# Kernel tuning notes

Measured on AMD Instinct MI355X. Metric: run time of the kernel, lower is better.

Reference implementation:

```python
import jax, jax.numpy as jnp
import numpy as np

TOPK = 8
N_EXPERTS = 64
ROUTE_SCALE = 1.0


def setup_inputs() -> dict:
    key = jax.random.key(0)
    k1, k2 = jax.random.split(key)
    x = jax.random.normal(k1, (16, 256, 64, 64), dtype=jnp.float32)
    gate_w = jax.random.normal(k2, (64, 256, 3, 3), dtype=jnp.float32) * 0.02  # [E, C, kh, kw]
    bias = jnp.zeros((64,), dtype=jnp.float32)  # load-balancing bias buffer
    return {"x": x, "gate_w": gate_w, "bias": bias}


def reference(x, gate_w, bias):
    # 3x3 conv, stride 1, pad 1 (SAME), no conv bias -> expert logits [B, E, H, W]
    logits = jax.lax.conv_general_dilated(
        x, gate_w, window_strides=(1, 1), padding="SAME",
        dimension_numbers=("NCHW", "OIHW", "NCHW"))
    scores = jax.nn.sigmoid(logits)                 # [B, E, H, W]
    s = jnp.moveaxis(scores, 1, -1)                 # [B, H, W, E]
    biased = s + bias                               # bias broadcast over experts
    _, idx = jax.lax.top_k(biased, TOPK)            # [B, H, W, K] (topk on biased scores)
    w = jnp.take_along_axis(s, idx, axis=-1)        # gather UNbiased scores
    w = jax.nn.softmax(w, axis=-1) * ROUTE_SCALE    # softmax over the K selected experts
    weights = jnp.moveaxis(w, -1, 1)                # [B, K, H, W] to match torch layout
    indices = jnp.moveaxis(idx, -1, 1)              # [B, K, H, W]
    counts = jnp.zeros((N_EXPERTS,), jnp.int32).at[idx.ravel()].add(1)  # bincount
    return weights, indices, counts
```

## Files before the change

### kernel.cpp

```cpp
#include <hip/hip_runtime.h>


typedef _Float16 half8 __attribute__((ext_vector_type(8)));
typedef __attribute__((ext_vector_type(4))) float f32x4;

#define LOG2E 1.44269504f

__device__ __forceinline__ unsigned short f2h_bits(float f) {
    _Float16 h = (_Float16)f;
    unsigned short b;
    __builtin_memcpy(&b, &h, 2);
    return b;
}

constexpr int WB_U4 = 8 * 9 * 4 * 64;

__global__ __launch_bounds__(256) void gate_prep(const float* __restrict__ gw,
                                                 unsigned short* __restrict__ wB,
                                                 float* __restrict__ out) {
    int g = blockIdx.x * 256 + threadIdx.x;
    if (blockIdx.x == 0 && threadIdx.x < 64) out[1048576 + threadIdx.x] = 0.f;
    if (g >= WB_U4) return;
    int lane = g & 63;
    int nt   = (g >> 6) & 3;
    int rest = g >> 8;
    int t = rest % 9, q = rest / 9;
    int e  = nt * 16 + (lane & 15);
    int c0 = q * 32 + (lane >> 4) * 8;
    unsigned short o[8];
#pragma unroll
    for (int j = 0; j < 8; ++j)
        o[j] = f2h_bits(gw[(e * 256 + c0 + j) * 9 + t]);
    uint4 pk;
    pk.x = (unsigned)o[0] | ((unsigned)o[1] << 16);
    pk.y = (unsigned)o[2] | ((unsigned)o[3] << 16);
    pk.z = (unsigned)o[4] | ((unsigned)o[5] << 16);
    pk.w = (unsigned)o[6] | ((unsigned)o[7] << 16);
    ((uint4*)wB)[g] = pk;
}

constexpr int CSTR = 40;
constexpr int SLAB = 3 * 66 * CSTR;
constexpr int SSTR = 68;

__global__ __launch_bounds__(256, 4) void gate_main(
    const float* __restrict__ x, const float* __restrict__ bias,
    const unsigned short* __restrict__ wB, float* __restrict__ out) {
    __shared__ unsigned short xs[2 * SLAB];
    __shared__ float bias_s[64];
    __shared__ int   hist[64];

    const int tid  = threadIdx.x;
    const int lane = tid & 63;
    const int rw   = tid >> 6;
    const int blk  = blockIdx.x;
    const int b    = blk & 15;
    const int r    = blk >> 4;

    if (tid < 64) { bias_s[tid] = bias[tid]; hist[tid] = 0; }

    {
        uint4 z = {0u, 0u, 0u, 0u};
        uint4* p = (uint4*)xs;
#pragma unroll
        for (int i = 0; i < 8; ++i) {
            int idx = tid + i * 256;
            if (idx < 2 * SLAB / 8) p[idx] = z;
        }
    }

    bool tOk[4];
    int  tSrc[4], tDst[4];
#pragma unroll
    for (int i = 0; i < 4; ++i) {
        int T = tid + i * 256;
        bool ex = (T < 792);
        int chh = T / 198, s = T - chh * 198;
        int row2 = s / 66, wp = s - row2 * 66;
        int gr = r - 1 + row2, gwc = wp - 1;
        tOk[i]  = ex && (gr >= 0) && (gr < 64) && (gwc >= 0) && (gwc < 64);
        tSrc[i] = ((b * 256 + chh * 8) * 64 + gr) * 64 + gwc;
        tDst[i] = (row2 * 66 + wp) * CSTR + chh * 8;
    }

    float tb[4][8];
    auto issueT = [&](int i, int dq) {
        if (tOk[i]) {
            const float* p = x + tSrc[i] + dq * 131072;
#pragma unroll
            for (int u = 0; u < 8; ++u) tb[i][u] = p[u * 4096];
        }
    };
    auto commitT = [&](int i, unsigned short* dst) {
        if (tOk[i]) {
            uint4 pk;
            pk.x = (unsigned)f2h_bits(tb[i][0]) | ((unsigned)f2h_bits(tb[i][1]) << 16);
            pk.y = (unsigned)f2h_bits(tb[i][2]) | ((unsigned)f2h_bits(tb[i][3]) << 16);
            pk.z = (unsigned)f2h_bits(tb[i][4]) | ((unsigned)f2h_bits(tb[i][5]) << 16);
            pk.w = (unsigned)f2h_bits(tb[i][6]) | ((unsigned)f2h_bits(tb[i][7]) << 16);
            *(uint4*)(dst + tDst[i]) = pk;
        }
    };

    const int ph = rw >> 1, eh = rw & 1;
    half8 Aa[3][2];
    uint4 Bb[3][2];
    auto prefA = [&](const unsigned short* buf, int t, int slot) {
        const int kh = t / 3, kw = t % 3;
        const unsigned short* abase =
            buf + (kh * 66 + ph * 32 + (lane & 15) + kw) * CSTR + (lane >> 4) * 8;
#pragma unroll
        for (int mt = 0; mt < 2; ++mt)
            Aa[slot][mt] = *(const half8*)(abase + mt * 16 * CSTR);
    };
    auto prefB = [&](int T9, int slot) {
        const uint4* bp = (const uint4*)wB + (T9 * 4 + eh * 2) * 64 + lane;
#pragma unroll
        for (int nt = 0; nt < 2; ++nt) Bb[slot][nt] = bp[nt * 64];
    };

    f32x4 acc[2][2];
#pragma unroll
    for (int mt = 0; mt < 2; ++mt)
#pragma unroll
        for (int nt = 0; nt < 2; ++nt) acc[mt][nt] = (f32x4){0.f, 0.f, 0.f, 0.f};

    auto mfma_tap = [&](int slot) {
#pragma unroll
        for (int nt = 0; nt < 2; ++nt) {
            half8 bfr;
            __builtin_memcpy(&bfr, &Bb[slot][nt], 16);
#pragma unroll
            for (int mt = 0; mt < 2; ++mt)
                acc[mt][nt] = __builtin_amdgcn_mfma_f32_16x16x32_f16(
                    Aa[slot][mt], bfr, acc[mt][nt], 0, 0, 0);
        }
    };

    __syncthreads();

    issueT(0, 0); issueT(1, 0); issueT(2, 0); issueT(3, 0);
    commitT(0, xs); commitT(1, xs); commitT(2, xs); commitT(3, xs);
    issueT(0, 1); issueT(1, 1); issueT(2, 1); issueT(3, 1);
    prefB(0, 0); prefB(1, 1); prefB(2, 2);
    __syncthreads();

#pragma unroll 1
    for (int q = 0; q < 8; ++q) {
        const unsigned short* cur = xs + (q & 1) * SLAB;
        unsigned short*       nxt = xs + ((q + 1) & 1) * SLAB;
        const int  T0  = q * 9;
        const bool cmt = (q < 7);
        const bool iss = (q < 6);

        prefA(cur, 0, 0); prefA(cur, 1, 1);
        if (cmt) { commitT(0, nxt); commitT(1, nxt); commitT(2, nxt); commitT(3, nxt); }
        mfma_tap(0); prefB(T0 + 3, 0); prefA(cur, 2, 2);
        mfma_tap(1); prefB(T0 + 4, 1); prefA(cur, 3, 0);
        mfma_tap(2); prefB(T0 + 5, 2); prefA(cur, 4, 1);
        mfma_tap(0); prefB(T0 + 6, 0); prefA(cur, 5, 2);
        mfma_tap(1); prefB(T0 + 7, 1); prefA(cur, 6, 0);
        mfma_tap(2); prefB(T0 + 8, 2); prefA(cur, 7, 1);
        __builtin_amdgcn_sched_barrier(0);
        if (iss) { issueT(0, q + 2); issueT(1, q + 2); issueT(2, q + 2); issueT(3, q + 2); }
        __builtin_amdgcn_sched_barrier(0);
        mfma_tap(0); if (cmt) prefB(T0 + 9, 0);  prefA(cur, 8, 2);
        mfma_tap(1); if (cmt) prefB(T0 + 10, 1);
        mfma_tap(2); if (cmt) prefB(T0 + 11, 2);
        __syncthreads();
    }

    float* scf = (float*)xs;
#pragma unroll
    for (int mt = 0; mt < 2; ++mt)
#pragma unroll
        for (int nt = 0; nt < 2; ++nt)
#pragma unroll
            for (int rr = 0; rr < 4; ++rr) {
                float v = acc[mt][nt][rr];
                float s = 1.f / (1.f + __builtin_amdgcn_exp2f(-v * LOG2E));
                int p = ph * 32 + mt * 16 + ((lane >> 4) << 2) + rr;
                int e = eh * 32 + nt * 16 + (lane & 15);
                scf[p * SSTR + e] = s;
            }
    __syncthreads();

    if (tid < 64) {
        const float* row = scf + tid * SSTR;
        float tv[8];
        int   ti[8];
#pragma unroll
        for (int k = 0; k < 8; ++k) { tv[k] = -3.0e38f; ti[k] = 0; }
#pragma unroll
        for (int j4 = 0; j4 < 16; ++j4) {
            f32x4 blkv = *(const f32x4*)(row + j4 * 4);
#pragma unroll
            for (int j = 0; j < 4; ++j) {
                int   e  = j4 * 4 + j;
                float bs = blkv[j] + bias_s[e];
                if (bs > tv[7]) {
                    tv[7] = bs; ti[7] = e;
#pragma unroll
                    for (int k = 7; k > 0; --k) {
                        float fa = tv[k - 1], fb = tv[k];
                        int   ia = ti[k - 1], ib = ti[k];
                        bool  sw = fb > fa;
                        tv[k - 1] = sw ? fb : fa; tv[k] = sw ? fa : fb;
                        ti[k - 1] = sw ? ib : ia; ti[k] = sw ? ia : ib;
                    }
                }
            }
        }
        float u[8], mx = -3.0e38f;
#pragma unroll
        for (int k = 0; k < 8; ++k) { u[k] = tv[k] - bias_s[ti[k]]; mx = fmaxf(mx, u[k]); }
        float ex[8], sum = 0.f;
#pragma unroll
        for (int k = 0; k < 8; ++k) { ex[k] = __builtin_amdgcn_exp2f((u[k] - mx) * LOG2E); sum += ex[k]; }
        float inv = 1.f / sum;

        int obase = b * 32768 + r * 64 + tid;
#pragma unroll
        for (int k = 0; k < 8; ++k) {
            out[obase + k * 4096]          = ex[k] * inv;
            out[524288 + obase + k * 4096] = (float)ti[k];
            atomicAdd(&hist[ti[k]], 1);
        }
    }
    __syncthreads();
    if (tid < 64) atomicAdd(out + 1048576 + tid, (float)hist[tid]);
}

extern "C" void kernel_launch(void* const* d_in, const int* in_sizes, int n_in,
                              void* d_out, int out_size, void* d_ws, size_t ws_size,
                              hipStream_t stream) {
    const float* x    = (const float*)d_in[0];
    const float* gw   = (const float*)d_in[1];
    const float* bias = (const float*)d_in[2];
    float* out = (float*)d_out;
    unsigned short* wB = (unsigned short*)d_ws;

    gate_prep<<<72, 256, 0, stream>>>(gw, wB, out);
    gate_main<<<1024, 256, 0, stream>>>(x, bias, wB, out);
}
```

Before: 142.7 us.

## Pre-transpose input to padded NHWC fp16 and stream conv operands from global

Adds a prep kernel that converts x once into a zero-padded channel-last fp16 buffer in workspace, alongside the weight packing. The new main kernel reads MFMA A-fragments straight from this global buffer, so there is no LDS staging, no per-block fp32-to-fp16 conversion and no per-slab barriers. This costs an extra full pass writing and reading a roughly 36 MB intermediate, and the input is re-read for each of the three kernel rows with reuse left to cache. The fallback path is kept for small workspaces and spreads its LDS commits between MFMA taps.

```diff
diff --git a/kernel.cpp b/kernel.cpp
--- a/kernel.cpp
+++ b/kernel.cpp
@@ -14,6 +14,210 @@
 }
 
 constexpr int WB_U4 = 8 * 9 * 4 * 64;
+constexpr size_t XT_BYTES = (size_t)16 * 66 * 66 * 256 * 2;
+constexpr size_t WS_NEED  = XT_BYTES + (size_t)WB_U4 * 16 + 65536;
+
+
+constexpr int NB_INT = 4096, NB_BOR = 65, NB_WB = 72;
+constexpr int PREP_GRID = NB_INT + NB_BOR + NB_WB;
+
+__global__ __launch_bounds__(256) void prep_all(
+    const float* __restrict__ x, const float* __restrict__ gw,
+    _Float16* __restrict__ xT, unsigned short* __restrict__ wB,
+    float* __restrict__ out) {
+    const int blk = blockIdx.x, tid = threadIdx.x;
+    if (blk < NB_INT) {
+        int gid = blk * 256 + tid;
+        int w = gid & 63, c16 = (gid >> 6) & 15, h = (gid >> 10) & 63, b = gid >> 16;
+        int c0 = c16 * 16;
+        const float* src = x + ((b * 256 + c0) * 64 + h) * 64 + w;
+        float v[16];
+#pragma unroll
+        for (int j = 0; j < 16; ++j) v[j] = src[j * 4096];
+        uint4 p0, p1;
+        p0.x = (unsigned)f2h_bits(v[0])  | ((unsigned)f2h_bits(v[1])  << 16);
+        p0.y = (unsigned)f2h_bits(v[2])  | ((unsigned)f2h_bits(v[3])  << 16);
+        p0.z = (unsigned)f2h_bits(v[4])  | ((unsigned)f2h_bits(v[5])  << 16);
+        p0.w = (unsigned)f2h_bits(v[6])  | ((unsigned)f2h_bits(v[7])  << 16);
+        p1.x = (unsigned)f2h_bits(v[8])  | ((unsigned)f2h_bits(v[9])  << 16);
+        p1.y = (unsigned)f2h_bits(v[10]) | ((unsigned)f2h_bits(v[11]) << 16);
+        p1.z = (unsigned)f2h_bits(v[12]) | ((unsigned)f2h_bits(v[13]) << 16);
+        p1.w = (unsigned)f2h_bits(v[14]) | ((unsigned)f2h_bits(v[15]) << 16);
+        int site = (b * 66 + h + 1) * 66 + (w + 1);
+        uint4* dst = (uint4*)xT + site * 32 + c16 * 2;
+        dst[0] = p0; dst[1] = p1;
+    } else if (blk < NB_INT + NB_BOR) {
+        int t = (blk - NB_INT) * 256 + tid;
+        int site = t >> 2, part = t & 3;
+        int sb = site / 260, s = site - sb * 260;
+        int hp, wp;
+        if (s < 132) { hp = (s >= 66) ? 65 : 0; wp = (s >= 66) ? (s - 66) : s; }
+        else         { int s2 = s - 132; hp = 1 + (s2 >> 1); wp = (s2 & 1) * 65; }
+        uint4 z = {0u, 0u, 0u, 0u};
+        uint4* dst = (uint4*)xT + ((sb * 66 + hp) * 66 + wp) * 32 + part * 8;
+#pragma unroll
+        for (int k = 0; k < 8; ++k) dst[k] = z;
+    } else {
+        int wblk = blk - (NB_INT + NB_BOR);
+        if (wblk == 0 && tid < 64) out[1048576 + tid] = 0.f;
+        int g = wblk * 256 + tid;
+        int lane = g & 63;
+        int nt   = (g >> 6) & 3;
+        int rest = g >> 8;
+        int t = rest % 9, q = rest / 9;
+        int e  = nt * 16 + (lane & 15);
+        int c0 = q * 32 + (lane >> 4) * 8;
+        unsigned short o[8];
+#pragma unroll
+        for (int j = 0; j < 8; ++j)
+            o[j] = f2h_bits(gw[(e * 256 + c0 + j) * 9 + t]);
+        uint4 pk;
+        pk.x = (unsigned)o[0] | ((unsigned)o[1] << 16);
+        pk.y = (unsigned)o[2] | ((unsigned)o[3] << 16);
+        pk.z = (unsigned)o[4] | ((unsigned)o[5] << 16);
+        pk.w = (unsigned)o[6] | ((unsigned)o[7] << 16);
+        ((uint4*)wB)[g] = pk;
+    }
+}
+
+constexpr int SSTR = 68;
+
+__global__ __launch_bounds__(256, 4) void gate_main2(
+    const _Float16* __restrict__ xT, const float* __restrict__ bias,
+    const unsigned short* __restrict__ wB, float* __restrict__ out) {
+    __shared__ float scf[64 * SSTR];
+    __shared__ float bias_s[64];
+    __shared__ int   hist[64];
+
+    const int tid  = threadIdx.x;
+    const int lane = tid & 63;
+    const int rw   = tid >> 6;
+    const int blk  = blockIdx.x;
+    const int b    = blk & 15;
+    const int r    = blk >> 4;
+
+    if (tid < 64) { bias_s[tid] = bias[tid]; hist[tid] = 0; }
+
+    const int ph = rw >> 1, eh = rw & 1;
+
+    const _Float16* pa[3][2];
+#pragma unroll
+    for (int kh = 0; kh < 3; ++kh)
+#pragma unroll
+        for (int m = 0; m < 2; ++m)
+            pa[kh][m] = xT + (size_t)(((b * 66 + r + kh) * 66) +
+                              ph * 32 + m * 16 + (lane & 15)) * 256 + (lane >> 4) * 8;
+
+    const uint4* bptr = (const uint4*)wB + eh * 128 + lane;
+
+    half8 Aa[3][2];
+    uint4 Bb[3][2];
+    f32x4 acc[2][2];
+#pragma unroll
+    for (int mt = 0; mt < 2; ++mt)
+#pragma unroll
+        for (int nt = 0; nt < 2; ++nt) acc[mt][nt] = (f32x4){0.f, 0.f, 0.f, 0.f};
+
+    auto LD = [&](int t, int slot) {
+        const int kh = t / 3, kw = t % 3;
+#pragma unroll
+        for (int m = 0; m < 2; ++m)
+            Aa[slot][m] = *(const half8*)(pa[kh][m] + kw * 256);
+#pragma unroll
+        for (int nt = 0; nt < 2; ++nt) Bb[slot][nt] = bptr[nt * 64];
+        bptr += 256;
+    };
+    auto mfma_tap = [&](int slot) {
+#pragma unroll
+        for (int nt = 0; nt < 2; ++nt) {
+            half8 bfr;
+            __builtin_memcpy(&bfr, &Bb[slot][nt], 16);
+#pragma unroll
+            for (int mt = 0; mt < 2; ++mt)
+                acc[mt][nt] = __builtin_amdgcn_mfma_f32_16x16x32_f16(
+                    Aa[slot][mt], bfr, acc[mt][nt], 0, 0, 0);
+        }
+    };
+
+    LD(0, 0); LD(1, 1); LD(2, 2);
+
+#pragma unroll 1
+    for (int q = 0; q < 8; ++q) {
+        mfma_tap(0); LD(3, 0);
+        mfma_tap(1); LD(4, 1);
+        mfma_tap(2); LD(5, 2);
+        mfma_tap(0); LD(6, 0);
+        mfma_tap(1); LD(7, 1);
+        mfma_tap(2); LD(8, 2);
+#pragma unroll
+        for (int kh = 0; kh < 3; ++kh)
+#pragma unroll
+            for (int m = 0; m < 2; ++m) pa[kh][m] += 32;
+        mfma_tap(0); LD(0, 0);
+        mfma_tap(1); LD(1, 1);
+        mfma_tap(2); LD(2, 2);
+    }
+
+#pragma unroll
+    for (int mt = 0; mt < 2; ++mt)
+#pragma unroll
+        for (int nt = 0; nt < 2; ++nt)
+#pragma unroll
+            for (int rr = 0; rr < 4; ++rr) {
+                float v = acc[mt][nt][rr];
+                float s = 1.f / (1.f + __builtin_amdgcn_exp2f(-v * LOG2E));
+                int p = ph * 32 + mt * 16 + ((lane >> 4) << 2) + rr;
+                int e = eh * 32 + nt * 16 + (lane & 15);
+                scf[p * SSTR + e] = s;
+            }
+    __syncthreads();
+
+    if (tid < 64) {
+        const float* row = scf + tid * SSTR;
+        float tv[8];
+        int   ti[8];
+#pragma unroll
+        for (int k = 0; k < 8; ++k) { tv[k] = -3.0e38f; ti[k] = 0; }
+#pragma unroll
+        for (int j4 = 0; j4 < 16; ++j4) {
+            f32x4 blkv = *(const f32x4*)(row + j4 * 4);
+#pragma unroll
+            for (int j = 0; j < 4; ++j) {
+                int   e  = j4 * 4 + j;
+                float bs = blkv[j] + bias_s[e];
+                if (bs > tv[7]) {
+                    tv[7] = bs; ti[7] = e;
+#pragma unroll
+                    for (int k = 7; k > 0; --k) {
+                        float fa = tv[k - 1], fb = tv[k];
+                        int   ia = ti[k - 1], ib = ti[k];
+                        bool  sw = fb > fa;
+                        tv[k - 1] = sw ? fb : fa; tv[k] = sw ? fa : fb;
+                        ti[k - 1] = sw ? ib : ia; ti[k] = sw ? ia : ib;
+                    }
+                }
+            }
+        }
+        float u[8], mx = -3.0e38f;
+#pragma unroll
+        for (int k = 0; k < 8; ++k) { u[k] = tv[k] - bias_s[ti[k]]; mx = fmaxf(mx, u[k]); }
+        float ex[8], sum = 0.f;
+#pragma unroll
+        for (int k = 0; k < 8; ++k) { ex[k] = __builtin_amdgcn_exp2f((u[k] - mx) * LOG2E); sum += ex[k]; }
+        float inv = 1.f / sum;
+
+        int obase = b * 32768 + r * 64 + tid;
+#pragma unroll
+        for (int k = 0; k < 8; ++k) {
+            out[obase + k * 4096]          = ex[k] * inv;
+            out[524288 + obase + k * 4096] = (float)ti[k];
+            atomicAdd(&hist[ti[k]], 1);
+        }
+    }
+    __syncthreads();
+    if (tid < 64) atomicAdd(out + 1048576 + tid, (float)hist[tid]);
+}
+
 
 __global__ __launch_bounds__(256) void gate_prep(const float* __restrict__ gw,
                                                  unsigned short* __restrict__ wB,
@@ -41,9 +245,8 @@
 
 constexpr int CSTR = 40;
 constexpr int SLAB = 3 * 66 * CSTR;
-constexpr int SSTR = 68;
-
-__global__ __launch_bounds__(256, 4) void gate_main(
+
+__global__ __launch_bounds__(256, 4) void gate_main_fb(
     const float* __restrict__ x, const float* __restrict__ bias,
     const unsigned short* __restrict__ wB, float* __restrict__ out) {
     __shared__ unsigned short xs[2 * SLAB];
@@ -58,7 +261,6 @@
     const int r    = blk >> 4;
 
     if (tid < 64) { bias_s[tid] = bias[tid]; hist[tid] = 0; }
-
     {
         uint4 z = {0u, 0u, 0u, 0u};
         uint4* p = (uint4*)xs;
@@ -138,7 +340,6 @@
     };
 
     __syncthreads();
-
     issueT(0, 0); issueT(1, 0); issueT(2, 0); issueT(3, 0);
     commitT(0, xs); commitT(1, xs); commitT(2, xs); commitT(3, xs);
     issueT(0, 1); issueT(1, 1); issueT(2, 1); issueT(3, 1);
@@ -154,11 +355,12 @@
         const bool iss = (q < 6);
 
         prefA(cur, 0, 0); prefA(cur, 1, 1);
-        if (cmt) { commitT(0, nxt); commitT(1, nxt); commitT(2, nxt); commitT(3, nxt); }
         mfma_tap(0); prefB(T0 + 3, 0); prefA(cur, 2, 2);
         mfma_tap(1); prefB(T0 + 4, 1); prefA(cur, 3, 0);
+        if (cmt) { commitT(0, nxt); commitT(1, nxt); }
         mfma_tap(2); prefB(T0 + 5, 2); prefA(cur, 4, 1);
         mfma_tap(0); prefB(T0 + 6, 0); prefA(cur, 5, 2);
+        if (cmt) { commitT(2, nxt); commitT(3, nxt); }
         mfma_tap(1); prefB(T0 + 7, 1); prefA(cur, 6, 0);
         mfma_tap(2); prefB(T0 + 8, 2); prefA(cur, 7, 1);
         __builtin_amdgcn_sched_barrier(0);
@@ -170,7 +372,7 @@
         __syncthreads();
     }
 
-    float* scf = (float*)xs;
+    float* scf2 = (float*)xs;
 #pragma unroll
     for (int mt = 0; mt < 2; ++mt)
 #pragma unroll
@@ -181,12 +383,12 @@
                 float s = 1.f / (1.f + __builtin_amdgcn_exp2f(-v * LOG2E));
                 int p = ph * 32 + mt * 16 + ((lane >> 4) << 2) + rr;
                 int e = eh * 32 + nt * 16 + (lane & 15);
-                scf[p * SSTR + e] = s;
+                scf2[p * SSTR + e] = s;
             }
     __syncthreads();
 
     if (tid < 64) {
-        const float* row = scf + tid * SSTR;
+        const float* row = scf2 + tid * SSTR;
         float tv[8];
         int   ti[8];
 #pragma unroll
@@ -238,8 +440,15 @@
     const float* gw   = (const float*)d_in[1];
     const float* bias = (const float*)d_in[2];
     float* out = (float*)d_out;
-    unsigned short* wB = (unsigned short*)d_ws;
-
-    gate_prep<<<72, 256, 0, stream>>>(gw, wB, out);
-    gate_main<<<1024, 256, 0, stream>>>(x, bias, wB, out);
-}
+
+    if (ws_size >= WS_NEED) {
+        _Float16* xT = (_Float16*)d_ws;
+        unsigned short* wB = (unsigned short*)((char*)d_ws + XT_BYTES);
+        prep_all<<<PREP_GRID, 256, 0, stream>>>(x, gw, xT, wB, out);
+        gate_main2<<<1024, 256, 0, stream>>>(xT, bias, wB, out);
+    } else {
+        unsigned short* wB = (unsigned short*)d_ws;
+        gate_prep<<<72, 256, 0, stream>>>(gw, wB, out);
+        gate_main_fb<<<1024, 256, 0, stream>>>(x, bias, wB, out);
+    }
+}
```

Result: slower. 226.8 us (+58.9%).
